# Optimization experiments

Hardware: AMD Instinct MI355X
Metric: run time of the kernel (lower is better)

## Reference

```python
import jax, jax.numpy as jnp
import numpy as np

N, E, V_H = 8192, 4096, 128
H0, H1 = 64, 1
BN_EPS = 1e-5


def _xavier(key, shape, gain=0.1):
    fan_in, fan_out = shape
    a = gain * np.sqrt(6.0 / (fan_in + fan_out))
    return jax.random.uniform(key, shape, jnp.float32, -a, a)


def setup_inputs() -> dict:
    key = jax.random.key(0)
    ks = jax.random.split(key, 8)
    X = jax.random.normal(ks[0], (N, V_H), jnp.float32)
    # incidence matrix: sparse-ish 0/1 pattern, stored dense as in the original
    H = (jax.random.uniform(ks[1], (N, E)) < 0.01).astype(jnp.float32)
    Dv_inv = jax.random.uniform(ks[2], (N,), jnp.float32, 0.05, 1.0)
    De_inv = jax.random.uniform(ks[3], (E,), jnp.float32, 0.05, 1.0)
    W = jax.random.uniform(ks[4], (E,), jnp.float32, 0.05, 1.0)
    theta1 = _xavier(ks[5], (V_H, H0))
    theta2 = _xavier(ks[6], (H0, H1))
    gamma = jnp.ones((H0,), jnp.float32)
    beta = jnp.zeros((H0,), jnp.float32)
    return {"X": X, "Dv_inv": Dv_inv, "De_inv": De_inv, "H": H, "W": W,
            "theta1": theta1, "theta2": theta2, "gamma": gamma, "beta": beta}


def reference(X, Dv_inv, De_inv, H, W, theta1, theta2, gamma, beta):
    # diag-matrix matmuls expressed as broadcast scaling (same math)
    # A = diag(Dv_inv) @ H @ diag(W) @ diag(De_inv)   -> [N, E]
    A = (Dv_inv[:, None] * H) * (W * De_inv)[None, :]

    def propagate(I_theta):
        # step2 @ diag(Dv_inv) @ I_theta, computed as A @ (H^T @ (Dv_inv * I_theta))
        # avoids materializing the [N, N] propagation matrix
        M = H.T @ (Dv_inv[:, None] * I_theta)  # [E, h]
        return A @ M                            # [N, h]

    Xbar1 = propagate(X @ theta1)
    X1 = jax.nn.leaky_relu(Xbar1, negative_slope=0.01)
    # BatchNorm1d in training mode (biased variance), momentum irrelevant for output
    mu = jnp.mean(X1, axis=0)
    var = jnp.var(X1, axis=0)
    X1 = (X1 - mu) / jnp.sqrt(var + BN_EPS) * gamma + beta

    Xbar2 = propagate(X1 @ theta2)
    return jax.nn.sigmoid(Xbar2).squeeze()  # [N]
```

## Files before the change

kernel.cpp:

```cpp
#include <hip/hip_runtime.h>
#include <hip/hip_bf16.h>
#include <math.h>

#define N_V   8192
#define N_E   4096
#define V_HID 128
#define H0_   64
#define CAP   96
#define CAPC  144
#define BN_EPS 1e-5f

typedef unsigned short u16;
typedef unsigned int   u32;
typedef unsigned long long u64;

__global__ __launch_bounds__(256) void k1_proj(const float* __restrict__ X, const float* __restrict__ th1,
                                               const float* __restrict__ Dv, float* __restrict__ P,
                                               float* __restrict__ zero_region) {
    int tid = threadIdx.x;
    if (blockIdx.x < 20) zero_region[blockIdx.x * 256 + tid] = 0.f;
    __shared__ float Th[V_HID][H0_];
    __shared__ float Xs[16][V_HID];
    int n0 = blockIdx.x * 16;
    for (int i = tid; i < 2048; i += 256) {
        float4 f = ((const float4*)th1)[i];
        int b = 4 * i;
        Th[b >> 6][(b & 63) + 0] = f.x;
        Th[b >> 6][(b & 63) + 1] = f.y;
        Th[b >> 6][(b & 63) + 2] = f.z;
        Th[b >> 6][(b & 63) + 3] = f.w;
    }
    for (int i = tid; i < 512; i += 256) {
        float4 f = ((const float4*)(X + (size_t)n0 * V_HID))[i];
        int b = 4 * i;
        Xs[b >> 7][(b & 127) + 0] = f.x;
        Xs[b >> 7][(b & 127) + 1] = f.y;
        Xs[b >> 7][(b & 127) + 2] = f.z;
        Xs[b >> 7][(b & 127) + 3] = f.w;
    }
    __syncthreads();
    int h = tid & 63, g = tid >> 6;
    int r0 = g * 4;
    float a0 = 0.f, a1 = 0.f, a2 = 0.f, a3 = 0.f;
    for (int k = 0; k < V_HID; ++k) {
        float t = Th[k][h];
        a0 += t * Xs[r0 + 0][k];
        a1 += t * Xs[r0 + 1][k];
        a2 += t * Xs[r0 + 2][k];
        a3 += t * Xs[r0 + 3][k];
    }
    P[(size_t)(n0 + r0 + 0) * H0_ + h] = Dv[n0 + r0 + 0] * a0;
    P[(size_t)(n0 + r0 + 1) * H0_ + h] = Dv[n0 + r0 + 1] * a1;
    P[(size_t)(n0 + r0 + 2) * H0_ + h] = Dv[n0 + r0 + 2] * a2;
    P[(size_t)(n0 + r0 + 3) * H0_ + h] = Dv[n0 + r0 + 3] * a3;
}

__global__ __launch_bounds__(256) void k2a_scan(const float* __restrict__ Hf,
                                                u32* __restrict__ nzlist, u32* __restrict__ nzcnt,
                                                u32* __restrict__ colcnt, u32* __restrict__ colentry) {
    __shared__ u32 rowbuf[4][CAP];
    int tid = threadIdx.x;
    int lane = tid & 63, wv = tid >> 6;
    int n = blockIdx.x * 4 + wv;
    const uint4* hrow4 = (const uint4*)(Hf + (size_t)n * N_E);
    u64 ltmask = (lane == 63) ? 0x7FFFFFFFFFFFFFFFull : ((1ull << lane) - 1ull);
    uint4 q[16];
#pragma unroll
    for (int m = 0; m < 16; ++m)
        q[m] = hrow4[m * 64 + lane];
    u32 cnt = 0;
#pragma unroll
    for (int m = 0; m < 16; ++m) {
        int ebase = (m * 64 + lane) * 4;
        u32 words[4] = { q[m].x, q[m].y, q[m].z, q[m].w };
#pragma unroll
        for (int j = 0; j < 4; ++j) {
            bool has = (words[j] & 0x7FFFFFFFu) != 0u;
            u64 bal = __ballot(has);
            if (bal) {
                if (has) {
                    u32 slot = cnt + (u32)__popcll(bal & ltmask);
                    if (slot < CAP) rowbuf[wv][slot] = (u32)(ebase + j);
                }
                cnt += (u32)__popcll(bal);
            }
        }
    }
    if (cnt > CAP) cnt = CAP;
    if (lane == 0) nzcnt[n] = cnt;
    for (u32 i = lane; i < cnt; i += 64) {
        u32 e = rowbuf[wv][i];
        nzlist[(size_t)n * CAP + i] = e;
        u32 cs = atomicAdd(&colcnt[e], 1u);
        if (cs < CAPC) colentry[(size_t)e * CAPC + cs] = (u32)n;
    }
}

__global__ __launch_bounds__(256) void k2b_gather(const u32* __restrict__ colcnt, const u32* __restrict__ colentry,
                                                  const float* __restrict__ P, const float* __restrict__ W,
                                                  const float* __restrict__ De, float* __restrict__ Mp) {
    int lane = threadIdx.x & 63;
    int e = blockIdx.x * 4 + (threadIdx.x >> 6);
    u32 cw = colcnt[e];
    int cnt = cw < CAPC ? (int)cw : CAPC;
    const u32* ce = colentry + (size_t)e * CAPC;
    float acc0 = 0.f, acc1 = 0.f;
    int i = 0;
    for (; i + 8 <= cnt; i += 8) {
        uint4 a = *((const uint4*)(ce + i));
        uint4 b = *((const uint4*)(ce + i + 4));
        float p0 = P[(a.x & (N_V - 1)) * H0_ + lane];
        float p1 = P[(a.y & (N_V - 1)) * H0_ + lane];
        float p2 = P[(a.z & (N_V - 1)) * H0_ + lane];
        float p3 = P[(a.w & (N_V - 1)) * H0_ + lane];
        float p4 = P[(b.x & (N_V - 1)) * H0_ + lane];
        float p5 = P[(b.y & (N_V - 1)) * H0_ + lane];
        float p6 = P[(b.z & (N_V - 1)) * H0_ + lane];
        float p7 = P[(b.w & (N_V - 1)) * H0_ + lane];
        acc0 += (p0 + p1) + (p2 + p3);
        acc1 += (p4 + p5) + (p6 + p7);
    }
    for (; i < cnt; ++i)
        acc0 += P[(ce[i] & (N_V - 1)) * H0_ + lane];
    Mp[(size_t)e * H0_ + lane] = W[e] * De[e] * (acc0 + acc1);
}

__global__ __launch_bounds__(256) void k3_layer1(const u32* __restrict__ nzlist, const u32* __restrict__ nzcnt,
                                                 const float* __restrict__ Mp, const float* __restrict__ Dv,
                                                 float* __restrict__ X1, float* __restrict__ bnp) {
    int lane = threadIdx.x & 63;
    int wv = threadIdx.x >> 6;
    int n = blockIdx.x * 4 + wv;
    const u32* lrow = nzlist + (size_t)n * CAP;
    u32 cw = nzcnt[n];
    int cnt = cw < CAP ? (int)cw : CAP;
    float acc0 = 0.f, acc1 = 0.f;
    int i = 0;
    for (; i + 8 <= cnt; i += 8) {
        uint4 a = *((const uint4*)(lrow + i));
        uint4 b = *((const uint4*)(lrow + i + 4));
        float p0 = Mp[(a.x & (N_E - 1)) * H0_ + lane];
        float p1 = Mp[(a.y & (N_E - 1)) * H0_ + lane];
        float p2 = Mp[(a.z & (N_E - 1)) * H0_ + lane];
        float p3 = Mp[(a.w & (N_E - 1)) * H0_ + lane];
        float p4 = Mp[(b.x & (N_E - 1)) * H0_ + lane];
        float p5 = Mp[(b.y & (N_E - 1)) * H0_ + lane];
        float p6 = Mp[(b.z & (N_E - 1)) * H0_ + lane];
        float p7 = Mp[(b.w & (N_E - 1)) * H0_ + lane];
        acc0 += (p0 + p1) + (p2 + p3);
        acc1 += (p4 + p5) + (p6 + p7);
    }
    for (; i < cnt; ++i)
        acc0 += Mp[(lrow[i] & (N_E - 1)) * H0_ + lane];
    float xb = Dv[n] * (acc0 + acc1);
    float x1 = xb > 0.f ? xb : 0.01f * xb;
    X1[(size_t)n * H0_ + lane] = x1;
    __shared__ float ssum[4][H0_], ssq[4][H0_];
    ssum[wv][lane] = x1;
    ssq[wv][lane] = x1 * x1;
    __syncthreads();
    if (wv == 0) {
        float a = ssum[0][lane] + ssum[1][lane] + ssum[2][lane] + ssum[3][lane];
        float b = ssq[0][lane] + ssq[1][lane] + ssq[2][lane] + ssq[3][lane];
        float* dst = bnp + (size_t)(blockIdx.x & 7) * 128;
        atomicAdd(&dst[lane], a);
        atomicAdd(&dst[64 + lane], b);
    }
}

__global__ __launch_bounds__(256) void k5_bn_proj(const float* __restrict__ X1, const float* __restrict__ bnp,
                                                  const float* __restrict__ gamma, const float* __restrict__ beta,
                                                  const float* __restrict__ th2, const float* __restrict__ Dv,
                                                  float* __restrict__ P2) {
    int lane = threadIdx.x & 63;
    int n = (int)((blockIdx.x * 256 + threadIdx.x) >> 6);
    float sum = 0.f, sq = 0.f;
#pragma unroll
    for (int p = 0; p < 8; ++p) { sum += bnp[p * 128 + lane]; sq += bnp[p * 128 + 64 + lane]; }
    float mu = sum * (1.f / N_V);
    float var = sq * (1.f / N_V) - mu * mu;
    float inv = rsqrtf(var + BN_EPS);
    float x = X1[(size_t)n * H0_ + lane];
    float xn = (x - mu) * inv * gamma[lane] + beta[lane];
    float t = xn * th2[lane];
#pragma unroll
    for (int off = 32; off > 0; off >>= 1) t += __shfl_xor(t, off);
    if (lane == 0) P2[n] = Dv[n] * t;
}

__global__ __launch_bounds__(256) void k6_edge2(const u32* __restrict__ colcnt, const u32* __restrict__ colentry,
                                                const float* __restrict__ P2, const float* __restrict__ W,
                                                const float* __restrict__ De, float* __restrict__ M2p) {
    int lane = threadIdx.x & 63;
    int e = blockIdx.x * 4 + (threadIdx.x >> 6);
    u32 cw = colcnt[e];
    int cnt = cw < CAPC ? (int)cw : CAPC;
    const u32* ce = colentry + (size_t)e * CAPC;
    float s = 0.f;
    for (int i = lane; i < cnt; i += 64)
        s += P2[ce[i] & (N_V - 1)];
#pragma unroll
    for (int off = 32; off > 0; off >>= 1) s += __shfl_xor(s, off);
    if (lane == 0) M2p[e] = W[e] * De[e] * s;
}

__global__ __launch_bounds__(256) void k7_out(const u32* __restrict__ nzlist, const u32* __restrict__ nzcnt,
                                              const float* __restrict__ M2p, const float* __restrict__ Dv,
                                              float* __restrict__ out) {
    int lane = threadIdx.x & 63;
    int n = blockIdx.x * 4 + (threadIdx.x >> 6);
    u32 cw = nzcnt[n];
    int cnt = cw < CAP ? (int)cw : CAP;
    const u32* lrow = nzlist + (size_t)n * CAP;
    float s = 0.f;
    for (int i = lane; i < cnt; i += 64)
        s += M2p[lrow[i] & (N_E - 1)];
#pragma unroll
    for (int off = 32; off > 0; off >>= 1) s += __shfl_xor(s, off);
    if (lane == 0) {
        float xb = Dv[n] * s;
        out[n] = 1.f / (1.f + expf(-xb));
    }
}

extern "C" void kernel_launch(void* const* d_in, const int* in_sizes, int n_in,
                              void* d_out, int out_size, void* d_ws, size_t ws_size,
                              hipStream_t stream) {
    const float* X   = (const float*)d_in[0];
    const float* Dv  = (const float*)d_in[1];
    const float* De  = (const float*)d_in[2];
    const float* Hf  = (const float*)d_in[3];
    const float* W   = (const float*)d_in[4];
    const float* th1 = (const float*)d_in[5];
    const float* th2 = (const float*)d_in[6];
    const float* gm  = (const float*)d_in[7];
    const float* bt  = (const float*)d_in[8];

    char* ws = (char*)d_ws;
    u32*   colcnt   = (u32*)  (ws + 0);
    float* bnp      = (float*)(ws + 16384);
    u32*   nzcnt    = (u32*)  (ws + 20480);
    float* M2p      = (float*)(ws + 53248);
    float* P2       = (float*)(ws + 69632);
    float* P        = (float*)(ws + 102400);
    float* X1       = P;
    float* Mp       = (float*)(ws + 2199552);
    u32*   nzlist   = (u32*)  (ws + 3248128);
    u32*   colentry = (u32*)  (ws + 6393856);

    k1_proj<<<N_V / 16, 256, 0, stream>>>(X, th1, Dv, P, (float*)ws);
    k2a_scan<<<N_V / 4, 256, 0, stream>>>(Hf, nzlist, nzcnt, colcnt, colentry);
    k2b_gather<<<N_E / 4, 256, 0, stream>>>(colcnt, colentry, P, W, De, Mp);
    k3_layer1<<<N_V / 4, 256, 0, stream>>>(nzlist, nzcnt, Mp, Dv, X1, bnp);
    k5_bn_proj<<<N_V / 4, 256, 0, stream>>>(X1, bnp, gm, bt, th2, Dv, P2);
    k6_edge2<<<N_E / 4, 256, 0, stream>>>(colcnt, colentry, P2, W, De, M2p);
    k7_out<<<N_V / 4, 256, 0, stream>>>(nzlist, nzcnt, M2p, Dv, (float*)d_out);
}
```

Baseline: 257.0 us.

## Fuse BN-projection into edge gather by factoring affine BN through the sum

Removes the separate BatchNorm+theta2 projection kernel and instead gathers raw X1 rows (64 floats each) per hyperedge, weighted by Dv. The affine BN and theta2 dot product are applied once per edge, using the linearity of the sum with a separate Dv-sum term for the bias. This saves a kernel launch and the P2 round trip. In exchange, each edge entry now reads a full 64-float row instead of one scalar, so gather traffic grows sharply, roughly 8192*~41*256B versus a streaming read of X1.

```diff
diff --git a/kernel.cpp b/kernel.cpp
--- a/kernel.cpp
+++ b/kernel.cpp
@@ -168,40 +168,57 @@
     }
 }
 
-__global__ __launch_bounds__(256) void k5_bn_proj(const float* __restrict__ X1, const float* __restrict__ bnp,
-                                                  const float* __restrict__ gamma, const float* __restrict__ beta,
-                                                  const float* __restrict__ th2, const float* __restrict__ Dv,
-                                                  float* __restrict__ P2) {
-    int lane = threadIdx.x & 63;
-    int n = (int)((blockIdx.x * 256 + threadIdx.x) >> 6);
+__global__ __launch_bounds__(256) void k6_fused(const u32* __restrict__ colcnt, const u32* __restrict__ colentry,
+                                                const float* __restrict__ X1, const float* __restrict__ bnp,
+                                                const float* __restrict__ gamma, const float* __restrict__ beta,
+                                                const float* __restrict__ th2, const float* __restrict__ Dv,
+                                                const float* __restrict__ W, const float* __restrict__ De,
+                                                float* __restrict__ M2p) {
+    int lane = threadIdx.x & 63;
+    int e = blockIdx.x * 4 + (threadIdx.x >> 6);
     float sum = 0.f, sq = 0.f;
 #pragma unroll
     for (int p = 0; p < 8; ++p) { sum += bnp[p * 128 + lane]; sq += bnp[p * 128 + 64 + lane]; }
     float mu = sum * (1.f / N_V);
     float var = sq * (1.f / N_V) - mu * mu;
     float inv = rsqrtf(var + BN_EPS);
-    float x = X1[(size_t)n * H0_ + lane];
-    float xn = (x - mu) * inv * gamma[lane] + beta[lane];
-    float t = xn * th2[lane];
-#pragma unroll
-    for (int off = 32; off > 0; off >>= 1) t += __shfl_xor(t, off);
-    if (lane == 0) P2[n] = Dv[n] * t;
-}
-
-__global__ __launch_bounds__(256) void k6_edge2(const u32* __restrict__ colcnt, const u32* __restrict__ colentry,
-                                                const float* __restrict__ P2, const float* __restrict__ W,
-                                                const float* __restrict__ De, float* __restrict__ M2p) {
-    int lane = threadIdx.x & 63;
-    int e = blockIdx.x * 4 + (threadIdx.x >> 6);
+    float gi = inv * gamma[lane];
+    float wh = gi * th2[lane];
+    float ch = (beta[lane] - mu * gi) * th2[lane];
     u32 cw = colcnt[e];
     int cnt = cw < CAPC ? (int)cw : CAPC;
     const u32* ce = colentry + (size_t)e * CAPC;
-    float s = 0.f;
-    for (int i = lane; i < cnt; i += 64)
-        s += P2[ce[i] & (N_V - 1)];
-#pragma unroll
-    for (int off = 32; off > 0; off >>= 1) s += __shfl_xor(s, off);
-    if (lane == 0) M2p[e] = W[e] * De[e] * s;
+    float vacc0 = 0.f, vacc1 = 0.f, dsum = 0.f;
+    int i = 0;
+    for (; i + 8 <= cnt; i += 8) {
+        uint4 a = *((const uint4*)(ce + i));
+        uint4 b = *((const uint4*)(ce + i + 4));
+        u32 n0 = a.x & (N_V - 1), n1 = a.y & (N_V - 1), n2 = a.z & (N_V - 1), n3 = a.w & (N_V - 1);
+        u32 n4 = b.x & (N_V - 1), n5 = b.y & (N_V - 1), n6 = b.z & (N_V - 1), n7 = b.w & (N_V - 1);
+        float d0 = Dv[n0], d1 = Dv[n1], d2 = Dv[n2], d3 = Dv[n3];
+        float d4 = Dv[n4], d5 = Dv[n5], d6 = Dv[n6], d7 = Dv[n7];
+        float x0 = X1[n0 * H0_ + lane];
+        float x1 = X1[n1 * H0_ + lane];
+        float x2 = X1[n2 * H0_ + lane];
+        float x3 = X1[n3 * H0_ + lane];
+        float x4 = X1[n4 * H0_ + lane];
+        float x5 = X1[n5 * H0_ + lane];
+        float x6 = X1[n6 * H0_ + lane];
+        float x7 = X1[n7 * H0_ + lane];
+        vacc0 += d0 * x0 + d1 * x1 + d2 * x2 + d3 * x3;
+        vacc1 += d4 * x4 + d5 * x5 + d6 * x6 + d7 * x7;
+        dsum += ((d0 + d1) + (d2 + d3)) + ((d4 + d5) + (d6 + d7));
+    }
+    for (; i < cnt; ++i) {
+        u32 n = ce[i] & (N_V - 1);
+        float d = Dv[n];
+        vacc0 += d * X1[n * H0_ + lane];
+        dsum += d;
+    }
+    float t = (vacc0 + vacc1) * wh + dsum * ch;
+#pragma unroll
+    for (int off = 32; off > 0; off >>= 1) t += __shfl_xor(t, off);
+    if (lane == 0) M2p[e] = W[e] * De[e] * t;
 }
 
 __global__ __launch_bounds__(256) void k7_out(const u32* __restrict__ nzlist, const u32* __restrict__ nzcnt,
@@ -241,7 +258,6 @@
     float* bnp      = (float*)(ws + 16384);
     u32*   nzcnt    = (u32*)  (ws + 20480);
     float* M2p      = (float*)(ws + 53248);
-    float* P2       = (float*)(ws + 69632);
     float* P        = (float*)(ws + 102400);
     float* X1       = P;
     float* Mp       = (float*)(ws + 2199552);
@@ -252,7 +268,6 @@
     k2a_scan<<<N_V / 4, 256, 0, stream>>>(Hf, nzlist, nzcnt, colcnt, colentry);
     k2b_gather<<<N_E / 4, 256, 0, stream>>>(colcnt, colentry, P, W, De, Mp);
     k3_layer1<<<N_V / 4, 256, 0, stream>>>(nzlist, nzcnt, Mp, Dv, X1, bnp);
-    k5_bn_proj<<<N_V / 4, 256, 0, stream>>>(X1, bnp, gm, bt, th2, Dv, P2);
-    k6_edge2<<<N_E / 4, 256, 0, stream>>>(colcnt, colentry, P2, W, De, M2p);
+    k6_fused<<<N_E / 4, 256, 0, stream>>>(colcnt, colentry, X1, bnp, gm, bt, th2, Dv, W, De, M2p);
     k7_out<<<N_V / 4, 256, 0, stream>>>(nzlist, nzcnt, M2p, Dv, (float*)d_out);
 }
```

Result: slower. 265.3 us (+3.2%).

## Fuse all stages into one cooperative persistent kernel with grid syncs

Applied to the files above, without the earlier changes.

Replaces the seven separate kernel launches with one cooperative kernel that runs each stage as a grid-stride loop separated by grid-wide barriers. It also overlaps the incidence scan with the X·theta1 projection inside the same phase. The goal is to remove per-launch overhead and tail gaps between the small dependent kernels. The cost is six grid syncs and a grid capped at occupancy, and the old multi-kernel path is kept as a fallback.

```diff
diff --git a/kernel.cpp b/kernel.cpp
--- a/kernel.cpp
+++ b/kernel.cpp
@@ -1,6 +1,8 @@
 #include <hip/hip_runtime.h>
-#include <hip/hip_bf16.h>
+#include <hip/hip_cooperative_groups.h>
 #include <math.h>
+
+namespace cg = cooperative_groups;
 
 #define N_V   8192
 #define N_E   4096
@@ -10,9 +12,225 @@
 #define CAPC  144
 #define BN_EPS 1e-5f
 
-typedef unsigned short u16;
 typedef unsigned int   u32;
 typedef unsigned long long u64;
+
+__global__ __launch_bounds__(256) void mega(
+    const float* __restrict__ X, const float* __restrict__ Hf,
+    const float* __restrict__ Dv, const float* __restrict__ De,
+    const float* __restrict__ W, const float* __restrict__ th1,
+    const float* __restrict__ th2, const float* __restrict__ gm,
+    const float* __restrict__ bt, float* __restrict__ out,
+    u32* __restrict__ colcnt, float* __restrict__ bnp,
+    u32* __restrict__ nzcnt, float* __restrict__ M2p, float* __restrict__ P2v,
+    float* __restrict__ P, float* __restrict__ Mp,
+    u32* __restrict__ nzlist, u32* __restrict__ colentry)
+{
+    __shared__ __align__(16) char smem_raw[8192];
+    cg::grid_group gg = cg::this_grid();
+    const int tid  = threadIdx.x;
+    const int bid  = blockIdx.x;
+    const int G    = gridDim.x;
+    const int lane = tid & 63;
+    const int wv   = tid >> 6;
+
+    for (int idx = bid * 256 + tid; idx < 5120; idx += G * 256)
+        colcnt[idx] = 0u;
+    gg.sync();
+
+    {
+        u32* rowbuf = (u32*)smem_raw;
+        u64 ltmask = (lane == 63) ? 0x7FFFFFFFFFFFFFFFull : ((1ull << lane) - 1ull);
+        for (int g = bid; g < N_V / 4; g += G) {
+            int n = g * 4 + wv;
+            const uint4* hrow4 = (const uint4*)(Hf + (size_t)n * N_E);
+            uint4 q[16];
+#pragma unroll
+            for (int m = 0; m < 16; ++m)
+                q[m] = hrow4[m * 64 + lane];
+            u32 cnt = 0;
+#pragma unroll
+            for (int m = 0; m < 16; ++m) {
+                int ebase = (m * 64 + lane) * 4;
+                u32 words[4] = { q[m].x, q[m].y, q[m].z, q[m].w };
+#pragma unroll
+                for (int j = 0; j < 4; ++j) {
+                    bool has = (words[j] & 0x7FFFFFFFu) != 0u;
+                    u64 bal = __ballot(has);
+                    if (bal) {
+                        if (has) {
+                            u32 slot = cnt + (u32)__popcll(bal & ltmask);
+                            if (slot < CAP) rowbuf[wv * CAP + slot] = (u32)(ebase + j);
+                        }
+                        cnt += (u32)__popcll(bal);
+                    }
+                }
+            }
+            if (cnt > CAP) cnt = CAP;
+            if (lane == 0) nzcnt[n] = cnt;
+            for (u32 i = lane; i < cnt; i += 64) {
+                u32 e = rowbuf[wv * CAP + i];
+                nzlist[(size_t)n * CAP + i] = e;
+                u32 cs = atomicAdd(&colcnt[e], 1u);
+                if (cs < CAPC) colentry[(size_t)e * CAPC + cs] = (u32)n;
+            }
+        }
+    }
+
+    {
+        float (*Xs)[V_HID] = (float (*)[V_HID])smem_raw;
+        for (int t = bid; t < N_V / 16; t += G) {
+            __syncthreads();
+            const float4* xr = (const float4*)(X + (size_t)t * 16 * V_HID);
+            for (int i = tid; i < 512; i += 256) {
+                float4 f = xr[i];
+                int b = 4 * i;
+                Xs[b >> 7][(b & 127) + 0] = f.x;
+                Xs[b >> 7][(b & 127) + 1] = f.y;
+                Xs[b >> 7][(b & 127) + 2] = f.z;
+                Xs[b >> 7][(b & 127) + 3] = f.w;
+            }
+            __syncthreads();
+            int r0 = wv * 4;
+            float a0 = 0.f, a1 = 0.f, a2 = 0.f, a3 = 0.f;
+#pragma unroll 8
+            for (int k = 0; k < V_HID; ++k) {
+                float tt = th1[k * H0_ + lane];
+                a0 += tt * Xs[r0 + 0][k];
+                a1 += tt * Xs[r0 + 1][k];
+                a2 += tt * Xs[r0 + 2][k];
+                a3 += tt * Xs[r0 + 3][k];
+            }
+            int n0 = t * 16;
+            P[(size_t)(n0 + r0 + 0) * H0_ + lane] = Dv[n0 + r0 + 0] * a0;
+            P[(size_t)(n0 + r0 + 1) * H0_ + lane] = Dv[n0 + r0 + 1] * a1;
+            P[(size_t)(n0 + r0 + 2) * H0_ + lane] = Dv[n0 + r0 + 2] * a2;
+            P[(size_t)(n0 + r0 + 3) * H0_ + lane] = Dv[n0 + r0 + 3] * a3;
+        }
+    }
+    gg.sync();
+
+    for (int eg = bid; eg < N_E / 4; eg += G) {
+        int e = eg * 4 + wv;
+        u32 cw = colcnt[e];
+        int cnt = cw < CAPC ? (int)cw : CAPC;
+        const u32* ce = colentry + (size_t)e * CAPC;
+        float acc0 = 0.f, acc1 = 0.f;
+        int i = 0;
+        for (; i + 8 <= cnt; i += 8) {
+            uint4 a = *((const uint4*)(ce + i));
+            uint4 b = *((const uint4*)(ce + i + 4));
+            float p0 = P[(a.x & (N_V - 1)) * H0_ + lane];
+            float p1 = P[(a.y & (N_V - 1)) * H0_ + lane];
+            float p2 = P[(a.z & (N_V - 1)) * H0_ + lane];
+            float p3 = P[(a.w & (N_V - 1)) * H0_ + lane];
+            float p4 = P[(b.x & (N_V - 1)) * H0_ + lane];
+            float p5 = P[(b.y & (N_V - 1)) * H0_ + lane];
+            float p6 = P[(b.z & (N_V - 1)) * H0_ + lane];
+            float p7 = P[(b.w & (N_V - 1)) * H0_ + lane];
+            acc0 += (p0 + p1) + (p2 + p3);
+            acc1 += (p4 + p5) + (p6 + p7);
+        }
+        for (; i < cnt; ++i)
+            acc0 += P[(ce[i] & (N_V - 1)) * H0_ + lane];
+        Mp[(size_t)e * H0_ + lane] = W[e] * De[e] * (acc0 + acc1);
+    }
+    gg.sync();
+
+    {
+        float* ssum = (float*)smem_raw;
+        float* ssq  = ssum + 256;
+        for (int g = bid; g < N_V / 4; g += G) {
+            int n = g * 4 + wv;
+            const u32* lrow = nzlist + (size_t)n * CAP;
+            u32 cw = nzcnt[n];
+            int cnt = cw < CAP ? (int)cw : CAP;
+            float acc0 = 0.f, acc1 = 0.f;
+            int i = 0;
+            for (; i + 8 <= cnt; i += 8) {
+                uint4 a = *((const uint4*)(lrow + i));
+                uint4 b = *((const uint4*)(lrow + i + 4));
+                float p0 = Mp[(a.x & (N_E - 1)) * H0_ + lane];
+                float p1 = Mp[(a.y & (N_E - 1)) * H0_ + lane];
+                float p2 = Mp[(a.z & (N_E - 1)) * H0_ + lane];
+                float p3 = Mp[(a.w & (N_E - 1)) * H0_ + lane];
+                float p4 = Mp[(b.x & (N_E - 1)) * H0_ + lane];
+                float p5 = Mp[(b.y & (N_E - 1)) * H0_ + lane];
+                float p6 = Mp[(b.z & (N_E - 1)) * H0_ + lane];
+                float p7 = Mp[(b.w & (N_E - 1)) * H0_ + lane];
+                acc0 += (p0 + p1) + (p2 + p3);
+                acc1 += (p4 + p5) + (p6 + p7);
+            }
+            for (; i < cnt; ++i)
+                acc0 += Mp[(lrow[i] & (N_E - 1)) * H0_ + lane];
+            float xb = Dv[n] * (acc0 + acc1);
+            float x1 = xb > 0.f ? xb : 0.01f * xb;
+            P[(size_t)n * H0_ + lane] = x1;
+            ssum[wv * 64 + lane] = x1;
+            ssq [wv * 64 + lane] = x1 * x1;
+            __syncthreads();
+            if (wv == 0) {
+                float a = ssum[0 * 64 + lane] + ssum[1 * 64 + lane] + ssum[2 * 64 + lane] + ssum[3 * 64 + lane];
+                float b = ssq [0 * 64 + lane] + ssq [1 * 64 + lane] + ssq [2 * 64 + lane] + ssq [3 * 64 + lane];
+                float* dst = bnp + (size_t)(g & 7) * 128;
+                atomicAdd(&dst[lane], a);
+                atomicAdd(&dst[64 + lane], b);
+            }
+            __syncthreads();
+        }
+    }
+    gg.sync();
+
+    {
+        float sum = 0.f, sq = 0.f;
+#pragma unroll
+        for (int p = 0; p < 8; ++p) { sum += bnp[p * 128 + lane]; sq += bnp[p * 128 + 64 + lane]; }
+        float mu = sum * (1.f / N_V);
+        float var = sq * (1.f / N_V) - mu * mu;
+        float inv = rsqrtf(var + BN_EPS);
+        float gm_l = gm[lane], bt_l = bt[lane], th2_l = th2[lane];
+        for (int g = bid; g < N_V / 4; g += G) {
+            int n = g * 4 + wv;
+            float x = P[(size_t)n * H0_ + lane];
+            float xn = (x - mu) * inv * gm_l + bt_l;
+            float t = xn * th2_l;
+#pragma unroll
+            for (int off = 32; off > 0; off >>= 1) t += __shfl_xor(t, off);
+            if (lane == 0) P2v[n] = Dv[n] * t;
+        }
+    }
+    gg.sync();
+
+    for (int eg = bid; eg < N_E / 4; eg += G) {
+        int e = eg * 4 + wv;
+        u32 cw = colcnt[e];
+        int cnt = cw < CAPC ? (int)cw : CAPC;
+        const u32* ce = colentry + (size_t)e * CAPC;
+        float s = 0.f;
+        for (int i = lane; i < cnt; i += 64)
+            s += P2v[ce[i] & (N_V - 1)];
+#pragma unroll
+        for (int off = 32; off > 0; off >>= 1) s += __shfl_xor(s, off);
+        if (lane == 0) M2p[e] = W[e] * De[e] * s;
+    }
+    gg.sync();
+
+    for (int g = bid; g < N_V / 4; g += G) {
+        int n = g * 4 + wv;
+        u32 cw = nzcnt[n];
+        int cnt = cw < CAP ? (int)cw : CAP;
+        const u32* lrow = nzlist + (size_t)n * CAP;
+        float s = 0.f;
+        for (int i = lane; i < cnt; i += 64)
+            s += M2p[lrow[i] & (N_E - 1)];
+#pragma unroll
+        for (int off = 32; off > 0; off >>= 1) s += __shfl_xor(s, off);
+        if (lane == 0) {
+            float xb = Dv[n] * s;
+            out[n] = 1.f / (1.f + expf(-xb));
+        }
+    }
+}
 
 __global__ __launch_bounds__(256) void k1_proj(const float* __restrict__ X, const float* __restrict__ th1,
                                                const float* __restrict__ Dv, float* __restrict__ P,
@@ -223,6 +441,9 @@
     }
 }
 
+static int g_mode = 0;
+static int g_grid = 0;
+
 extern "C" void kernel_launch(void* const* d_in, const int* in_sizes, int n_in,
                               void* d_out, int out_size, void* d_ws, size_t ws_size,
                               hipStream_t stream) {
@@ -235,24 +456,51 @@
     const float* th2 = (const float*)d_in[6];
     const float* gm  = (const float*)d_in[7];
     const float* bt  = (const float*)d_in[8];
+    float* out = (float*)d_out;
 
     char* ws = (char*)d_ws;
     u32*   colcnt   = (u32*)  (ws + 0);
     float* bnp      = (float*)(ws + 16384);
     u32*   nzcnt    = (u32*)  (ws + 20480);
     float* M2p      = (float*)(ws + 53248);
-    float* P2       = (float*)(ws + 69632);
+    float* P2v      = (float*)(ws + 69632);
     float* P        = (float*)(ws + 102400);
-    float* X1       = P;
     float* Mp       = (float*)(ws + 2199552);
     u32*   nzlist   = (u32*)  (ws + 3248128);
     u32*   colentry = (u32*)  (ws + 6393856);
 
+    if (g_mode == 0) {
+        int dev = 0, coopAttr = 0, numCU = 0, nb = 0;
+        hipGetDevice(&dev);
+        hipDeviceGetAttribute(&coopAttr, hipDeviceAttributeCooperativeLaunch, dev);
+        hipDeviceGetAttribute(&numCU, hipDeviceAttributeMultiprocessorCount, dev);
+        hipError_t oe = hipOccupancyMaxActiveBlocksPerMultiprocessor(
+            &nb, reinterpret_cast<const void*>(mega), 256, 0);
+        if (coopAttr && oe == hipSuccess && nb >= 1 && numCU >= 1) {
+            long cap = (long)nb * (long)numCU;
+            g_grid = (int)(cap < 2048 ? cap : 2048);
+            g_mode = 1;
+        } else {
+            g_mode = 2;
+        }
+    }
+
+    if (g_mode == 1) {
+        void* args[] = { (void*)&X, (void*)&Hf, (void*)&Dv, (void*)&De, (void*)&W,
+                         (void*)&th1, (void*)&th2, (void*)&gm, (void*)&bt, (void*)&out,
+                         (void*)&colcnt, (void*)&bnp, (void*)&nzcnt, (void*)&M2p, (void*)&P2v,
+                         (void*)&P, (void*)&Mp, (void*)&nzlist, (void*)&colentry };
+        hipError_t err = hipLaunchCooperativeKernel((const void*)mega, dim3(g_grid),
+                                                    dim3(256), args, 0, stream);
+        if (err == hipSuccess) return;
+        g_mode = 2;
+    }
+
     k1_proj<<<N_V / 16, 256, 0, stream>>>(X, th1, Dv, P, (float*)ws);
     k2a_scan<<<N_V / 4, 256, 0, stream>>>(Hf, nzlist, nzcnt, colcnt, colentry);
     k2b_gather<<<N_E / 4, 256, 0, stream>>>(colcnt, colentry, P, W, De, Mp);
-    k3_layer1<<<N_V / 4, 256, 0, stream>>>(nzlist, nzcnt, Mp, Dv, X1, bnp);
-    k5_bn_proj<<<N_V / 4, 256, 0, stream>>>(X1, bnp, gm, bt, th2, Dv, P2);
-    k6_edge2<<<N_E / 4, 256, 0, stream>>>(colcnt, colentry, P2, W, De, M2p);
-    k7_out<<<N_V / 4, 256, 0, stream>>>(nzlist, nzcnt, M2p, Dv, (float*)d_out);
-}
+    k3_layer1<<<N_V / 4, 256, 0, stream>>>(nzlist, nzcnt, Mp, Dv, P , bnp);
+    k5_bn_proj<<<N_V / 4, 256, 0, stream>>>(P , bnp, gm, bt, th2, Dv, P2v);
+    k6_edge2<<<N_E / 4, 256, 0, stream>>>(colcnt, colentry, P2v, W, De, M2p);
+    k7_out<<<N_V / 4, 256, 0, stream>>>(nzlist, nzcnt, M2p, Dv, out);
+}
```

Result: slower. 596.0 us (+131.9%).

## Merge scan with projection and fuse second-layer edge/out kernels via scatter atomics

Applied to the files above, without the earlier changes.

The projection kernel is merged into the incidence-scan kernel as extra blocks in one grid, and th1 is now read from global memory instead of staged in shared memory. The second-layer edge gather and vertex gather are fused into one kernel: each edge scatters its value to member vertices with float atomics, and the last finishing block (found with a done counter) applies the sigmoid. Zeroing moves to a memset plus in-kernel clearing of the accumulator. This removes two launches and one gather pass, at the cost of atomic contention, nondeterministic float summation order, and a serial tail on the last block.

```diff
diff --git a/kernel.cpp b/kernel.cpp
--- a/kernel.cpp
+++ b/kernel.cpp
@@ -1,5 +1,4 @@
 #include <hip/hip_runtime.h>
-#include <hip/hip_bf16.h>
 #include <math.h>
 
 #define N_V   8192
@@ -10,89 +9,85 @@
 #define CAPC  144
 #define BN_EPS 1e-5f
 
-typedef unsigned short u16;
 typedef unsigned int   u32;
 typedef unsigned long long u64;
 
-__global__ __launch_bounds__(256) void k1_proj(const float* __restrict__ X, const float* __restrict__ th1,
-                                               const float* __restrict__ Dv, float* __restrict__ P,
-                                               float* __restrict__ zero_region) {
-    int tid = threadIdx.x;
-    if (blockIdx.x < 20) zero_region[blockIdx.x * 256 + tid] = 0.f;
-    __shared__ float Th[V_HID][H0_];
-    __shared__ float Xs[16][V_HID];
-    int n0 = blockIdx.x * 16;
-    for (int i = tid; i < 2048; i += 256) {
-        float4 f = ((const float4*)th1)[i];
-        int b = 4 * i;
-        Th[b >> 6][(b & 63) + 0] = f.x;
-        Th[b >> 6][(b & 63) + 1] = f.y;
-        Th[b >> 6][(b & 63) + 2] = f.z;
-        Th[b >> 6][(b & 63) + 3] = f.w;
-    }
-    for (int i = tid; i < 512; i += 256) {
-        float4 f = ((const float4*)(X + (size_t)n0 * V_HID))[i];
-        int b = 4 * i;
-        Xs[b >> 7][(b & 127) + 0] = f.x;
-        Xs[b >> 7][(b & 127) + 1] = f.y;
-        Xs[b >> 7][(b & 127) + 2] = f.z;
-        Xs[b >> 7][(b & 127) + 3] = f.w;
-    }
-    __syncthreads();
-    int h = tid & 63, g = tid >> 6;
-    int r0 = g * 4;
-    float a0 = 0.f, a1 = 0.f, a2 = 0.f, a3 = 0.f;
-    for (int k = 0; k < V_HID; ++k) {
-        float t = Th[k][h];
-        a0 += t * Xs[r0 + 0][k];
-        a1 += t * Xs[r0 + 1][k];
-        a2 += t * Xs[r0 + 2][k];
-        a3 += t * Xs[r0 + 3][k];
-    }
-    P[(size_t)(n0 + r0 + 0) * H0_ + h] = Dv[n0 + r0 + 0] * a0;
-    P[(size_t)(n0 + r0 + 1) * H0_ + h] = Dv[n0 + r0 + 1] * a1;
-    P[(size_t)(n0 + r0 + 2) * H0_ + h] = Dv[n0 + r0 + 2] * a2;
-    P[(size_t)(n0 + r0 + 3) * H0_ + h] = Dv[n0 + r0 + 3] * a3;
-}
-
-__global__ __launch_bounds__(256) void k2a_scan(const float* __restrict__ Hf,
-                                                u32* __restrict__ nzlist, u32* __restrict__ nzcnt,
-                                                u32* __restrict__ colcnt, u32* __restrict__ colentry) {
-    __shared__ u32 rowbuf[4][CAP];
-    int tid = threadIdx.x;
-    int lane = tid & 63, wv = tid >> 6;
-    int n = blockIdx.x * 4 + wv;
-    const uint4* hrow4 = (const uint4*)(Hf + (size_t)n * N_E);
-    u64 ltmask = (lane == 63) ? 0x7FFFFFFFFFFFFFFFull : ((1ull << lane) - 1ull);
-    uint4 q[16];
-#pragma unroll
-    for (int m = 0; m < 16; ++m)
-        q[m] = hrow4[m * 64 + lane];
-    u32 cnt = 0;
-#pragma unroll
-    for (int m = 0; m < 16; ++m) {
-        int ebase = (m * 64 + lane) * 4;
-        u32 words[4] = { q[m].x, q[m].y, q[m].z, q[m].w };
-#pragma unroll
-        for (int j = 0; j < 4; ++j) {
-            bool has = (words[j] & 0x7FFFFFFFu) != 0u;
-            u64 bal = __ballot(has);
-            if (bal) {
-                if (has) {
-                    u32 slot = cnt + (u32)__popcll(bal & ltmask);
-                    if (slot < CAP) rowbuf[wv][slot] = (u32)(ebase + j);
+__global__ __launch_bounds__(256) void kA_scan_proj(
+    const float* __restrict__ Hf, const float* __restrict__ X,
+    const float* __restrict__ th1, const float* __restrict__ Dv,
+    float* __restrict__ P,
+    u32* __restrict__ nzlist, u32* __restrict__ nzcnt,
+    u32* __restrict__ colcnt, u32* __restrict__ colentry)
+{
+    __shared__ __align__(16) char sm[8192];
+    const int tid  = threadIdx.x;
+    const int bid  = blockIdx.x;
+    const int lane = tid & 63;
+    const int wv   = tid >> 6;
+
+    if (bid < N_V / 4) {
+        u32* rowbuf = (u32*)sm;
+        int n = bid * 4 + wv;
+        const uint4* hrow4 = (const uint4*)(Hf + (size_t)n * N_E);
+        u64 ltmask = (lane == 63) ? 0x7FFFFFFFFFFFFFFFull : ((1ull << lane) - 1ull);
+        uint4 q[16];
+#pragma unroll
+        for (int m = 0; m < 16; ++m)
+            q[m] = hrow4[m * 64 + lane];
+        u32 cnt = 0;
+#pragma unroll
+        for (int m = 0; m < 16; ++m) {
+            int ebase = (m * 64 + lane) * 4;
+            u32 words[4] = { q[m].x, q[m].y, q[m].z, q[m].w };
+#pragma unroll
+            for (int j = 0; j < 4; ++j) {
+                bool has = (words[j] & 0x7FFFFFFFu) != 0u;
+                u64 bal = __ballot(has);
+                if (bal) {
+                    if (has) {
+                        u32 slot = cnt + (u32)__popcll(bal & ltmask);
+                        if (slot < CAP) rowbuf[wv * CAP + slot] = (u32)(ebase + j);
+                    }
+                    cnt += (u32)__popcll(bal);
                 }
-                cnt += (u32)__popcll(bal);
             }
         }
-    }
-    if (cnt > CAP) cnt = CAP;
-    if (lane == 0) nzcnt[n] = cnt;
-    for (u32 i = lane; i < cnt; i += 64) {
-        u32 e = rowbuf[wv][i];
-        nzlist[(size_t)n * CAP + i] = e;
-        u32 cs = atomicAdd(&colcnt[e], 1u);
-        if (cs < CAPC) colentry[(size_t)e * CAPC + cs] = (u32)n;
+        if (cnt > CAP) cnt = CAP;
+        if (lane == 0) nzcnt[n] = cnt;
+        for (u32 i = lane; i < cnt; i += 64) {
+            u32 e = rowbuf[wv * CAP + i];
+            nzlist[(size_t)n * CAP + i] = e;
+            u32 cs = atomicAdd(&colcnt[e], 1u);
+            if (cs < CAPC) colentry[(size_t)e * CAPC + cs] = (u32)n;
+        }
+    } else {
+        float (*Xs)[V_HID] = (float (*)[V_HID])sm;
+        int t  = bid - N_V / 4;
+        int n0 = t * 16;
+        const float4* xr = (const float4*)(X + (size_t)n0 * V_HID);
+        for (int i = tid; i < 512; i += 256) {
+            float4 f = xr[i];
+            int b = 4 * i;
+            Xs[b >> 7][(b & 127) + 0] = f.x;
+            Xs[b >> 7][(b & 127) + 1] = f.y;
+            Xs[b >> 7][(b & 127) + 2] = f.z;
+            Xs[b >> 7][(b & 127) + 3] = f.w;
+        }
+        __syncthreads();
+        int r0 = wv * 4;
+        float a0 = 0.f, a1 = 0.f, a2 = 0.f, a3 = 0.f;
+#pragma unroll 8
+        for (int k = 0; k < V_HID; ++k) {
+            float tt = th1[k * H0_ + lane];
+            a0 += tt * Xs[r0 + 0][k];
+            a1 += tt * Xs[r0 + 1][k];
+            a2 += tt * Xs[r0 + 2][k];
+            a3 += tt * Xs[r0 + 3][k];
+        }
+        P[(size_t)(n0 + r0 + 0) * H0_ + lane] = Dv[n0 + r0 + 0] * a0;
+        P[(size_t)(n0 + r0 + 1) * H0_ + lane] = Dv[n0 + r0 + 1] * a1;
+        P[(size_t)(n0 + r0 + 2) * H0_ + lane] = Dv[n0 + r0 + 2] * a2;
+        P[(size_t)(n0 + r0 + 3) * H0_ + lane] = Dv[n0 + r0 + 3] * a3;
     }
 }
 
@@ -171,8 +166,12 @@
 __global__ __launch_bounds__(256) void k5_bn_proj(const float* __restrict__ X1, const float* __restrict__ bnp,
                                                   const float* __restrict__ gamma, const float* __restrict__ beta,
                                                   const float* __restrict__ th2, const float* __restrict__ Dv,
-                                                  float* __restrict__ P2) {
+                                                  float* __restrict__ P2v, u32* __restrict__ acc_zero) {
     int lane = threadIdx.x & 63;
+    {
+        int idx = blockIdx.x * 256 + threadIdx.x;
+        if (idx < 8256) acc_zero[idx] = 0u;
+    }
     int n = (int)((blockIdx.x * 256 + threadIdx.x) >> 6);
     float sum = 0.f, sq = 0.f;
 #pragma unroll
@@ -185,41 +184,44 @@
     float t = xn * th2[lane];
 #pragma unroll
     for (int off = 32; off > 0; off >>= 1) t += __shfl_xor(t, off);
-    if (lane == 0) P2[n] = Dv[n] * t;
-}
-
-__global__ __launch_bounds__(256) void k6_edge2(const u32* __restrict__ colcnt, const u32* __restrict__ colentry,
-                                                const float* __restrict__ P2, const float* __restrict__ W,
-                                                const float* __restrict__ De, float* __restrict__ M2p) {
-    int lane = threadIdx.x & 63;
-    int e = blockIdx.x * 4 + (threadIdx.x >> 6);
+    if (lane == 0) P2v[n] = Dv[n] * t;
+}
+
+__global__ __launch_bounds__(256) void k67_out(const u32* __restrict__ colcnt, const u32* __restrict__ colentry,
+                                               const float* __restrict__ P2v, const float* __restrict__ W,
+                                               const float* __restrict__ De, const float* __restrict__ Dv,
+                                               float* __restrict__ acc, u32* __restrict__ done,
+                                               float* __restrict__ out) {
+    int tid = threadIdx.x;
+    int lane = tid & 63;
+    int e = blockIdx.x * 4 + (tid >> 6);
     u32 cw = colcnt[e];
     int cnt = cw < CAPC ? (int)cw : CAPC;
     const u32* ce = colentry + (size_t)e * CAPC;
     float s = 0.f;
     for (int i = lane; i < cnt; i += 64)
-        s += P2[ce[i] & (N_V - 1)];
+        s += P2v[ce[i] & (N_V - 1)];
 #pragma unroll
     for (int off = 32; off > 0; off >>= 1) s += __shfl_xor(s, off);
-    if (lane == 0) M2p[e] = W[e] * De[e] * s;
-}
-
-__global__ __launch_bounds__(256) void k7_out(const u32* __restrict__ nzlist, const u32* __restrict__ nzcnt,
-                                              const float* __restrict__ M2p, const float* __restrict__ Dv,
-                                              float* __restrict__ out) {
-    int lane = threadIdx.x & 63;
-    int n = blockIdx.x * 4 + (threadIdx.x >> 6);
-    u32 cw = nzcnt[n];
-    int cnt = cw < CAP ? (int)cw : CAP;
-    const u32* lrow = nzlist + (size_t)n * CAP;
-    float s = 0.f;
+    float m2 = W[e] * De[e] * s;
     for (int i = lane; i < cnt; i += 64)
-        s += M2p[lrow[i] & (N_E - 1)];
-#pragma unroll
-    for (int off = 32; off > 0; off >>= 1) s += __shfl_xor(s, off);
-    if (lane == 0) {
-        float xb = Dv[n] * s;
-        out[n] = 1.f / (1.f + expf(-xb));
+        atomicAdd(&acc[ce[i] & (N_V - 1)], m2);
+
+    __threadfence();
+    __syncthreads();
+    __shared__ int amLast;
+    if (tid == 0) {
+        u32 old = atomicAdd(done, 1u);
+        amLast = (old == (u32)(gridDim.x - 1));
+    }
+    __syncthreads();
+    if (amLast) {
+        __threadfence();
+        for (int n = tid; n < N_V; n += 256) {
+            float a = __hip_atomic_load(&acc[n], __ATOMIC_RELAXED, __HIP_MEMORY_SCOPE_AGENT);
+            float xb = Dv[n] * a;
+            out[n] = 1.f / (1.f + expf(-xb));
+        }
     }
 }
 
@@ -235,24 +237,26 @@
     const float* th2 = (const float*)d_in[6];
     const float* gm  = (const float*)d_in[7];
     const float* bt  = (const float*)d_in[8];
+    float* out = (float*)d_out;
 
     char* ws = (char*)d_ws;
     u32*   colcnt   = (u32*)  (ws + 0);
     float* bnp      = (float*)(ws + 16384);
-    u32*   nzcnt    = (u32*)  (ws + 20480);
-    float* M2p      = (float*)(ws + 53248);
-    float* P2       = (float*)(ws + 69632);
-    float* P        = (float*)(ws + 102400);
+    float* acc      = (float*)(ws + 20480);
+    u32*   done     = (u32*)  (ws + 53248);
+    u32*   nzcnt    = (u32*)  (ws + 53504);
+    float* P2v      = (float*)(ws + 86272);
+    float* P        = (float*)(ws + 131072);
     float* X1       = P;
-    float* Mp       = (float*)(ws + 2199552);
-    u32*   nzlist   = (u32*)  (ws + 3248128);
-    u32*   colentry = (u32*)  (ws + 6393856);
-
-    k1_proj<<<N_V / 16, 256, 0, stream>>>(X, th1, Dv, P, (float*)ws);
-    k2a_scan<<<N_V / 4, 256, 0, stream>>>(Hf, nzlist, nzcnt, colcnt, colentry);
+    float* Mp       = (float*)(ws + 2228224);
+    u32*   nzlist   = (u32*)  (ws + 3276800);
+    u32*   colentry = (u32*)  (ws + 6422528);
+
+    hipMemsetAsync(ws, 0, 20480, stream);
+    kA_scan_proj<<<N_V / 4 + N_V / 16, 256, 0, stream>>>(Hf, X, th1, Dv, P,
+                                                         nzlist, nzcnt, colcnt, colentry);
     k2b_gather<<<N_E / 4, 256, 0, stream>>>(colcnt, colentry, P, W, De, Mp);
     k3_layer1<<<N_V / 4, 256, 0, stream>>>(nzlist, nzcnt, Mp, Dv, X1, bnp);
-    k5_bn_proj<<<N_V / 4, 256, 0, stream>>>(X1, bnp, gm, bt, th2, Dv, P2);
-    k6_edge2<<<N_E / 4, 256, 0, stream>>>(colcnt, colentry, P2, W, De, M2p);
-    k7_out<<<N_V / 4, 256, 0, stream>>>(nzlist, nzcnt, M2p, Dv, (float*)d_out);
-}
+    k5_bn_proj<<<N_V / 4, 256, 0, stream>>>(X1, bnp, gm, bt, th2, Dv, P2v, (u32*)acc);
+    k67_out<<<N_E / 4, 256, 0, stream>>>(colcnt, colentry, P2v, W, De, Dv, acc, done, out);
+}
```

Result: slower. 332.2 us (+29.3%).
